# Kernel tuning notes

Measured on AMD Instinct MI355X. Metric: run time of the kernel, lower is better.

Reference implementation:

```python
import jax, jax.numpy as jnp
import numpy as np

B, S, D = 2, 2048, 2048
H = 16
HD = D // H  # 128
ROPE_THETA = 10000.0


def _rotate_half(x):
    # interleaved rotate: [-x2_0, x1_0, -x2_1, x1_1, ...]
    x1 = x[..., ::2]
    x2 = x[..., 1::2]
    return jnp.stack((-x2, x1), axis=-1).reshape(x.shape)


def _rope_cos_sin(seq_len, head_dim, dtype):
    inv_freq = 1.0 / (ROPE_THETA ** (jnp.arange(0, head_dim, 2, dtype=jnp.float32) / head_dim))
    pos = jnp.arange(seq_len, dtype=jnp.float32)
    freqs = pos[:, None] * inv_freq[None, :]          # [S, HD/2]
    angles = jnp.concatenate((freqs, freqs), axis=-1)  # [S, HD]  (matches torch.cat((freqs, freqs), -1))
    return jnp.cos(angles).astype(dtype), jnp.sin(angles).astype(dtype)


def setup_inputs() -> dict:
    key = jax.random.key(0)
    ks = jax.random.split(key, 5)
    scale = 1.0 / np.sqrt(D)
    return {
        "x": jax.random.normal(ks[0], (B, S, D), dtype=jnp.float32),
        "Wq": jax.random.normal(ks[1], (D, D), dtype=jnp.float32) * scale,
        "Wk": jax.random.normal(ks[2], (D, D), dtype=jnp.float32) * scale,
        "Wv": jax.random.normal(ks[3], (D, D), dtype=jnp.float32) * scale,
        "Wo": jax.random.normal(ks[4], (D, D), dtype=jnp.float32) * scale,
    }


def reference(x, Wq, Wk, Wv, Wo):
    b, s, d = x.shape
    # separate Q/K/V projections (no bias), reshape to [B, H, S, HD]
    def proj(W):
        return jnp.einsum('bsd,de->bse', x, W).reshape(b, s, H, HD).transpose(0, 2, 1, 3)
    q, k, v = proj(Wq), proj(Wk), proj(Wv)

    cos, sin = _rope_cos_sin(s, HD, q.dtype)  # [S, HD]
    cos = cos[None, None, :, :]
    sin = sin[None, None, :, :]
    q = q * cos + _rotate_half(q) * sin
    k = k * cos + _rotate_half(k) * sin

    # causal scaled dot-product attention
    scores = jnp.einsum('bhqd,bhkd->bhqk', q, k) / jnp.sqrt(jnp.asarray(HD, q.dtype))
    causal = jnp.tril(jnp.ones((s, s), dtype=bool))
    scores = jnp.where(causal[None, None, :, :], scores, jnp.asarray(-jnp.inf, scores.dtype))
    attn = jax.nn.softmax(scores, axis=-1)
    out = jnp.einsum('bhqk,bhkd->bhqd', attn, v)

    out = out.transpose(0, 2, 1, 3).reshape(b, s, d)
    return jnp.einsum('bsd,de->bse', out, Wo)
```

## Files before the change

kernel.cpp:

```cpp
#include <hip/hip_runtime.h>
#include <hip/hip_bf16.h>
#include <math.h>

typedef unsigned short u16;
typedef unsigned int u32;

#define Bz 2
#define Sz 2048
#define Dz 2048
#define Hz 16
#define HDz 128
#define Mz 4096

typedef __bf16 bf16x8 __attribute__((ext_vector_type(8)));
typedef float f32x4 __attribute__((ext_vector_type(4)));

__device__ __forceinline__ float bf2f(u16 h) {
    union { u32 u; float f; } x; x.u = ((u32)h) << 16; return x.f;
}
__device__ __forceinline__ u16 f2bf(float f) {
    union { float f; u32 u; } x; x.f = f;
    u32 u = x.u;
    return (u16)((u + 0x7FFFu + ((u >> 16) & 1u)) >> 16);
}
__device__ __forceinline__ u32 pack_bf16_trunc(float lo, float hi) {
    union { float f; u32 u; } a, b; a.f = lo; b.f = hi;
    return (a.u >> 16) | (b.u & 0xFFFF0000u);
}
__device__ __forceinline__ u32 pack_bf16_rn(float lo, float hi) {
    return (u32)f2bf(lo) | ((u32)f2bf(hi) << 16);
}
__device__ __forceinline__ float fexp2(float x) {
#if __has_builtin(__builtin_amdgcn_exp2f)
    return __builtin_amdgcn_exp2f(x);
#else
    return exp2f(x);
#endif
}
__device__ __forceinline__ void gl_lds16(const void* g, void* l) {
    __builtin_amdgcn_global_load_lds(
        (const __attribute__((address_space(1))) void*)g,
        (__attribute__((address_space(3))) void*)l, 16, 0, 0);
}

__global__ void cvt_f32_bf16(const float* __restrict__ src, u16* __restrict__ dst) {
    size_t i = (size_t)blockIdx.x * blockDim.x + threadIdx.x;
    float4 a = ((const float4*)src)[2 * i];
    float4 b = ((const float4*)src)[2 * i + 1];
    u16 r[8] = {f2bf(a.x), f2bf(a.y), f2bf(a.z), f2bf(a.w),
                f2bf(b.x), f2bf(b.y), f2bf(b.z), f2bf(b.w)};
    *(uint4*)(dst + 8 * i) = *(const uint4*)r;
}

__global__ void transpose_w(const float* __restrict__ W0, const float* __restrict__ W1,
                            const float* __restrict__ W2, const float* __restrict__ W3,
                            u16* __restrict__ Wt) {
    __shared__ u16 t[64][65];
    const float* src = (blockIdx.z == 0) ? W0 : (blockIdx.z == 1) ? W1
                     : (blockIdx.z == 2) ? W2 : W3;
    u16* dst = Wt + (size_t)blockIdx.z * (Dz * Dz);
    int x = blockIdx.x * 64, y = blockIdx.y * 64;
    int c = threadIdx.x & 63, rb = (threadIdx.x >> 6) * 16;
#pragma unroll
    for (int i = 0; i < 16; i++) {
        int r = rb + i;
        t[r][c] = f2bf(src[(size_t)(y + r) * Dz + x + c]);
    }
    __syncthreads();
#pragma unroll
    for (int i = 0; i < 16; i++) {
        int r = rb + i;
        dst[(size_t)(x + r) * Dz + y + c] = t[c][r];
    }
}

template <int MODE>
__global__ void gemm_bt(const u16* __restrict__ A, const u16* __restrict__ BtBase,
                        void* __restrict__ CBase) {
    const int z = blockIdx.z;
    const u16* Bt = BtBase + (size_t)z * (Dz * Dz);
    const int tid = threadIdx.x, lane = tid & 63, wave = tid >> 6;
    const int ln = lane & 15, qd = lane >> 4;
    const int m0 = blockIdx.y * 128, n0 = blockIdx.x * 128;

    __shared__ __align__(16) u16 As[128][64];
    __shared__ __align__(16) u16 Bs[128][64];

    f32x4 acc[4][4];
#pragma unroll
    for (int i = 0; i < 4; i++)
#pragma unroll
        for (int j = 0; j < 4; j++) acc[i][j] = (f32x4){0.f, 0.f, 0.f, 0.f};

    const int wm = (wave >> 1) * 64, wn = (wave & 1) * 64;
    const int lr8 = lane >> 3;
    const int bgo = (((lane & 7) ^ lr8) * 8);
    const int x7 = ln & 7;

    for (int k0 = 0; k0 < Dz; k0 += 64) {
        const u16* ga = A  + (size_t)(m0 + wave * 32 + lr8) * Dz + k0 + bgo;
        const u16* gb = Bt + (size_t)(n0 + wave * 32 + lr8) * Dz + k0 + bgo;
#pragma unroll
        for (int i = 0; i < 4; i++) {
            gl_lds16(ga + (size_t)(8 * i) * Dz, &As[wave * 32 + 8 * i][0]);
            gl_lds16(gb + (size_t)(8 * i) * Dz, &Bs[wave * 32 + 8 * i][0]);
        }
        __syncthreads();
#pragma unroll
        for (int kc = 0; kc < 2; kc++) {
            bf16x8 af[4], bff[4];
            const int cs = ((4 * kc + qd) ^ x7) * 8;
#pragma unroll
            for (int i = 0; i < 4; i++) {
                af[i]  = *(const bf16x8*)&As[wm + i * 16 + ln][cs];
                bff[i] = *(const bf16x8*)&Bs[wn + i * 16 + ln][cs];
            }
#pragma unroll
            for (int i = 0; i < 4; i++)
#pragma unroll
                for (int j = 0; j < 4; j++)
                    acc[i][j] = __builtin_amdgcn_mfma_f32_16x16x32_bf16(
                        af[i], bff[j], acc[i][j], 0, 0, 0);
        }
        __syncthreads();
    }

#pragma unroll
    for (int i = 0; i < 4; i++) {
#pragma unroll
        for (int j = 0; j < 4; j++) {
#pragma unroll
            for (int r = 0; r < 4; r++) {
                int row = m0 + wm + i * 16 + qd * 4 + r;
                int col = n0 + wn + j * 16 + ln;
                if (MODE == 0) {
                    ((float*)CBase)[(size_t)row * Dz + col] = acc[i][j][r];
                } else {
                    u16* C = (u16*)CBase + (size_t)z * ((size_t)Mz * Dz);
                    u16 hv = f2bf(acc[i][j][r]);
                    int bb = row >> 11, ss = row & 2047;
                    int hh = col >> 7, hd = col & 127;
                    if (z == 2)
                        C[((size_t)(bb * Hz + hh) * HDz + hd) * Sz + ss] = hv;
                    else
                        C[((size_t)(bb * Hz + hh) * Sz + ss) * HDz + hd] = hv;
                }
            }
        }
    }
}

__global__ void rope_kernel(u16* __restrict__ Q, u16* __restrict__ Kk) {
    u32 idx = blockIdx.x * blockDim.x + threadIdx.x;
    int isK = (idx >> 22) & 1;
    u16* T = isK ? Kk : Q;
    u32 p = idx & 0x3FFFFFu;
    int j = p & 63;
    int s = (p >> 6) & 2047;
    size_t base = (size_t)(p >> 6) * HDz + 2 * j;
    u32 u = *(u32*)(T + base);
    float x0 = bf2f((u16)(u & 0xFFFFu));
    float x1 = bf2f((u16)(u >> 16));
    int i0 = (2 * j) & 63;
    const float LG = 0.20762050593046017f;
    float f0 = exp2f(-LG * (float)i0);
    float f1 = exp2f(-LG * (float)(i0 + 1));
    float th0 = (float)s * f0, th1 = (float)s * f1;
    float s0, c0, s1, c1;
    sincosf(th0, &s0, &c0);
    sincosf(th1, &s1, &c1);
    float scl = isK ? 1.0f : 0.12751771218027603f;
    float y0 = (x0 * c0 - x1 * s0) * scl;
    float y1 = (x1 * c1 + x0 * s1) * scl;
    u32 outw = (u32)f2bf(y0) | ((u32)f2bf(y1) << 16);
    *(u32*)(T + base) = outw;
}

__global__ __launch_bounds__(256, 4)
void flash_attn(const u16* __restrict__ Q, const u16* __restrict__ Kk,
                const u16* __restrict__ Vt, u16* __restrict__ O) {
    const int tid = threadIdx.x, lane = tid & 63, wave = tid >> 6;
    const int ln = lane & 15, qd = lane >> 4;
    const int bh = blockIdx.x & 31;
    const int qt = 31 - (blockIdx.x >> 5);
    const int b = bh >> 4, h = bh & 15;
    const int q0 = qt * 64;
    const u16* Qh = Q  + (size_t)bh * Sz * HDz;
    const u16* Kh = Kk + (size_t)bh * Sz * HDz;
    const u16* Vh = Vt + (size_t)bh * HDz * Sz;

    __shared__ __align__(16) u16 Ks[64][128];
    __shared__ __align__(16) u16 Vs[144][64];

    for (int idx = tid; idx < 16 * 64; idx += 256) {
        int rr = idx >> 6, cc = idx & 63;
        Vs[128 + rr][cc] = (rr == 0) ? (u16)0x3F80 : (u16)0;
    }

    const int qabs = q0 + wave * 16 + ln;
    bf16x8 qf[4];
#pragma unroll
    for (int kc = 0; kc < 4; kc++) {
        uint4 t = *(const uint4*)(Qh + (size_t)qabs * HDz + kc * 32 + qd * 8);
        qf[kc] = *(const bf16x8*)&t;
    }

    float m_run = -INFINITY;
    f32x4 oa[9];
#pragma unroll
    for (int n = 0; n < 9; n++) oa[n] = (f32x4){0.f, 0.f, 0.f, 0.f};

    const int x7 = ln & 7;
    const int l4 = lane >> 4, c16 = lane & 15;
    const int lr8 = lane >> 3;
    const int bgv = ((lane & 7) ^ lr8) * 8;

    for (int k0 = 0; k0 <= q0; k0 += 64) {
        {
#pragma unroll
            for (int i = 0; i < 4; i++) {
                int rw = 4 * (i & 1) + l4;
                const u16* gk = Kh + (size_t)(k0 + 16 * wave + 4 * i + l4) * HDz
                                   + ((c16 ^ rw) * 8);
                gl_lds16(gk, &Ks[16 * wave + 4 * i][0]);
            }
            const u16* gv = Vh + (size_t)(32 * wave + lr8) * Sz + k0 + bgv;
#pragma unroll
            for (int i = 0; i < 4; i++)
                gl_lds16(gv + (size_t)(8 * i) * Sz, &Vs[32 * wave + 8 * i][0]);
        }
        __syncthreads();

        f32x4 sc4[4];
#pragma unroll
        for (int mt = 0; mt < 4; mt++) sc4[mt] = (f32x4){0.f, 0.f, 0.f, 0.f};
#pragma unroll
        for (int kc = 0; kc < 4; kc++) {
            const int cs = ((4 * kc + qd) ^ x7) * 8;
#pragma unroll
            for (int mt = 0; mt < 4; mt++) {
                bf16x8 kf = *(const bf16x8*)&Ks[mt * 16 + ln][cs];
                sc4[mt] = __builtin_amdgcn_mfma_f32_16x16x32_bf16(kf, qf[kc], sc4[mt], 0, 0, 0);
            }
        }
        if (k0 == q0) {
#pragma unroll
            for (int mt = 0; mt < 4; mt++)
#pragma unroll
                for (int r = 0; r < 4; r++)
                    if (mt * 16 + qd * 4 + r > 16 * wave + ln) sc4[mt][r] = -3e38f;
        }

        float rm = -3e38f;
#pragma unroll
        for (int mt = 0; mt < 4; mt++) {
            rm = fmaxf(rm, fmaxf(fmaxf(sc4[mt][0], sc4[mt][1]),
                                 fmaxf(sc4[mt][2], sc4[mt][3])));
        }
        rm = fmaxf(rm, __shfl_xor(rm, 16));
        rm = fmaxf(rm, __shfl_xor(rm, 32));
        float mn = fmaxf(m_run, rm);
        bool resc = (__ballot(mn > m_run) != 0ULL);
        float al = fexp2(m_run - mn);
        m_run = mn;
        if (resc) {
#pragma unroll
            for (int n = 0; n < 9; n++)
#pragma unroll
                for (int r = 0; r < 4; r++) oa[n][r] *= al;
        }

        u32 pku[8];
#pragma unroll
        for (int mt = 0; mt < 4; mt++) {
#pragma unroll
            for (int t = 0; t < 2; t++)
                pku[mt * 2 + t] = pack_bf16_trunc(fexp2(sc4[mt][2 * t] - mn),
                                                  fexp2(sc4[mt][2 * t + 1] - mn));
        }

#pragma unroll
        for (int kc = 0; kc < 2; kc++) {
            union { u32 w[4]; bf16x8 v; } pb;
#pragma unroll
            for (int s = 0; s < 4; s++) {
                int srcl = ((2 * (qd & 1) + (s >> 1)) << 4) | ln;
                u32 a0 = (u32)__shfl((int)pku[4 * kc + (s & 1)], srcl);
                u32 a1 = (u32)__shfl((int)pku[4 * kc + 2 + (s & 1)], srcl);
                pb.w[s] = (qd & 2) ? a1 : a0;
            }
            const int cs = ((4 * kc + qd) ^ x7) * 8;
#pragma unroll
            for (int mt = 0; mt < 9; mt++) {
                bf16x8 vf = *(const bf16x8*)&Vs[mt * 16 + ln][cs];
                oa[mt] = __builtin_amdgcn_mfma_f32_16x16x32_bf16(vf, pb.v, oa[mt], 0, 0, 0);
            }
        }
        __syncthreads();
    }

    float l = __shfl(oa[8][0], ln);
    float linv = 1.0f / l;
    u16* op = O + ((size_t)b * Sz + qabs) * Dz + h * HDz;
#pragma unroll
    for (int mt = 0; mt < 8; mt++) {
        u32 w0 = pack_bf16_rn(oa[mt][0] * linv, oa[mt][1] * linv);
        u32 w1 = pack_bf16_rn(oa[mt][2] * linv, oa[mt][3] * linv);
        uint2 ww; ww.x = w0; ww.y = w1;
        *(uint2*)(op + mt * 16 + qd * 4) = ww;
    }
}

extern "C" void kernel_launch(void* const* d_in, const int* in_sizes, int n_in,
                              void* d_out, int out_size, void* d_ws, size_t ws_size,
                              hipStream_t stream) {
    const float* x  = (const float*)d_in[0];
    const float* Wq = (const float*)d_in[1];
    const float* Wk = (const float*)d_in[2];
    const float* Wv = (const float*)d_in[3];
    const float* Wo = (const float*)d_in[4];
    u16* ws  = (u16*)d_ws;

    u16* wt = ws;
    u16* q  = ws + 16777216;
    u16* kk = q + 8388608;
    u16* v  = kk + 8388608;
    u16* xb = v + 8388608;
    u16* o  = xb;

    cvt_f32_bf16<<<dim3(4096), 256, 0, stream>>>(x, xb);
    transpose_w<<<dim3(32, 32, 4), 256, 0, stream>>>(Wq, Wk, Wv, Wo, wt);
    gemm_bt<1><<<dim3(16, 32, 3), 256, 0, stream>>>(xb, wt, q);
    rope_kernel<<<dim3(32768), 256, 0, stream>>>(q, kk);
    flash_attn<<<dim3(1024), 256, 0, stream>>>(q, kk, v, o);
    gemm_bt<0><<<dim3(16, 32, 1), 256, 0, stream>>>(o, wt + 3 * 4194304, (float*)d_out);
}
```

Measured before the change: 373.4 us.

## Use 256x256-tile 8-wave pipelined GEMM for the QKV projection

Replaces the QKV projection GEMM with a new kernel that uses 256x256 output tiles, 512 threads, and double-buffered LDS filled by direct global-to-LDS loads. The main loop is split into eight phases that interleave the next stage's loads with MFMA work, using explicit waitcnt, barriers and setprio. The goal is more data reuse per tile and better overlap of memory with compute. In exchange it uses more LDS and registers, and the launch grid shrinks to 384 blocks.

```diff
diff --git a/kernel.cpp b/kernel.cpp
--- a/kernel.cpp
+++ b/kernel.cpp
@@ -145,6 +145,123 @@
                     else
                         C[((size_t)(bb * Hz + hh) * Sz + ss) * HDz + hd] = hv;
                 }
+            }
+        }
+    }
+}
+
+#define G256_STAGE_A(BUF, MH, KOFS) do {                                        \
+    gl_lds16(gA0 + (size_t)(MH) * 64 * Dz + (KOFS), &As[BUF][sa0 + (MH) * 64][0]); \
+    gl_lds16(gA1 + (size_t)(MH) * 64 * Dz + (KOFS), &As[BUF][sa1 + (MH) * 64][0]); \
+} while (0)
+#define G256_STAGE_B(BUF, NH, KOFS) do {                                        \
+    gl_lds16(gB0 + (size_t)(NH) * 32 * Dz + (KOFS), &Bs[BUF][sb0 + (NH) * 32][0]); \
+    gl_lds16(gB1 + (size_t)(NH) * 32 * Dz + (KOFS), &Bs[BUF][sb1 + (NH) * 32][0]); \
+} while (0)
+#define G256_NOVM do {} while (0)
+#define G256_VM4  asm volatile("s_waitcnt vmcnt(4)" ::: "memory")
+#define G256_PHASE(BUF, MH, NH, STG, VMW) do {                                  \
+    bf16x8 af[4][2], bfr[2][2];                                                 \
+    _Pragma("unroll")                                                           \
+    for (int kc = 0; kc < 2; ++kc) {                                            \
+        const int cs = ((4 * kc + qd) ^ x7) * 8;                                \
+        _Pragma("unroll")                                                       \
+        for (int m = 0; m < 4; ++m)                                             \
+            af[m][kc] = *(const bf16x8*)&As[BUF][wr * 128 + (MH) * 64 + m * 16 + ln][cs]; \
+        _Pragma("unroll")                                                       \
+        for (int n = 0; n < 2; ++n)                                             \
+            bfr[n][kc] = *(const bf16x8*)&Bs[BUF][wc * 64 + (NH) * 32 + n * 16 + ln][cs]; \
+    }                                                                           \
+    STG;                                                                        \
+    asm volatile("s_waitcnt lgkmcnt(8)" ::: "memory");                          \
+    asm volatile("s_barrier" ::: "memory");                                     \
+    asm volatile("s_waitcnt lgkmcnt(0)" ::: "memory");                          \
+    __builtin_amdgcn_sched_barrier(0);                                          \
+    __builtin_amdgcn_s_setprio(1);                                              \
+    _Pragma("unroll")                                                           \
+    for (int kc = 0; kc < 2; ++kc)                                              \
+        _Pragma("unroll")                                                       \
+        for (int m = 0; m < 4; ++m)                                             \
+            _Pragma("unroll")                                                   \
+            for (int n = 0; n < 2; ++n)                                         \
+                acc[(MH) * 4 + m][(NH) * 2 + n] =                               \
+                    __builtin_amdgcn_mfma_f32_16x16x32_bf16(                    \
+                        af[m][kc], bfr[n][kc],                                  \
+                        acc[(MH) * 4 + m][(NH) * 2 + n], 0, 0, 0);              \
+    __builtin_amdgcn_s_setprio(0);                                              \
+    VMW;                                                                        \
+    asm volatile("s_barrier" ::: "memory");                                     \
+} while (0)
+
+__global__ __launch_bounds__(512, 2)
+void gemm256_qkv(const u16* __restrict__ A, const u16* __restrict__ BtBase,
+                 u16* __restrict__ CBase) {
+    const int z = blockIdx.z;
+    const u16* Bt = BtBase + (size_t)z * (Dz * Dz);
+    const int tid = threadIdx.x, lane = tid & 63, w = tid >> 6;
+    const int ln = lane & 15, qd = lane >> 4;
+    const int x7 = ln & 7;
+    const int wr = w >> 2, wc = w & 3;
+    const int m0 = blockIdx.y * 256, n0 = blockIdx.x * 256;
+
+    __shared__ __align__(16) u16 As[2][256][64];
+    __shared__ __align__(16) u16 Bs[2][256][64];
+
+    f32x4 acc[8][4];
+#pragma unroll
+    for (int i = 0; i < 8; ++i)
+#pragma unroll
+        for (int j = 0; j < 4; ++j) acc[i][j] = (f32x4){0.f, 0.f, 0.f, 0.f};
+
+    const int l8 = lane >> 3;
+    const int cblk = ((lane & 7) ^ l8) * 8;
+    const int sa0 = ((w >= 4) ? 128 : 0) + (((2 * w) & 7) * 8);
+    const int sa1 = ((w >= 4) ? 128 : 0) + (((2 * w + 1) & 7) * 8);
+    const int sb0 = (w >> 1) * 64 + (((2 * w) & 3) * 8);
+    const int sb1 = (w >> 1) * 64 + (((2 * w + 1) & 3) * 8);
+    const u16* gA0 = A + (size_t)(m0 + sa0 + l8) * Dz + cblk;
+    const u16* gA1 = A + (size_t)(m0 + sa1 + l8) * Dz + cblk;
+    const u16* gB0 = Bt + (size_t)(n0 + sb0 + l8) * Dz + cblk;
+    const u16* gB1 = Bt + (size_t)(n0 + sb1 + l8) * Dz + cblk;
+
+    G256_STAGE_A(0, 0, 0); G256_STAGE_A(0, 1, 0);
+    G256_STAGE_B(0, 0, 0); G256_STAGE_B(0, 1, 0);
+    G256_STAGE_A(1, 0, 64); G256_STAGE_B(1, 0, 64);
+    asm volatile("s_waitcnt vmcnt(4)" ::: "memory");
+    asm volatile("s_barrier" ::: "memory");
+
+#pragma unroll 1
+    for (int it = 0; it < Dz / 128; ++it) {
+        const int kb = it * 128;
+        const int k1 = kb + 64;
+        const int k2 = (kb + 128 < Dz) ? (kb + 128) : (Dz - 128);
+        const int k3 = (kb + 192 < Dz) ? (kb + 192) : (Dz - 64);
+        G256_PHASE(0, 0, 0, G256_STAGE_A(1, 1, k1), G256_NOVM);
+        G256_PHASE(0, 0, 1, G256_STAGE_B(1, 1, k1), G256_NOVM);
+        G256_PHASE(0, 1, 0, G256_STAGE_A(0, 0, k2), G256_NOVM);
+        G256_PHASE(0, 1, 1, G256_STAGE_B(0, 0, k2), G256_VM4);
+        G256_PHASE(1, 0, 0, G256_STAGE_A(0, 1, k2), G256_NOVM);
+        G256_PHASE(1, 0, 1, G256_STAGE_B(0, 1, k2), G256_NOVM);
+        G256_PHASE(1, 1, 0, G256_STAGE_A(1, 0, k3), G256_NOVM);
+        G256_PHASE(1, 1, 1, G256_STAGE_B(1, 0, k3), G256_VM4);
+    }
+
+    u16* C = CBase + (size_t)z * ((size_t)Mz * Dz);
+#pragma unroll
+    for (int i = 0; i < 8; ++i) {
+#pragma unroll
+        for (int j = 0; j < 4; ++j) {
+#pragma unroll
+            for (int r = 0; r < 4; ++r) {
+                int row = m0 + wr * 128 + i * 16 + qd * 4 + r;
+                int col = n0 + wc * 64 + j * 16 + ln;
+                u16 hv = f2bf(acc[i][j][r]);
+                int bb = row >> 11, ss = row & 2047;
+                int hh = col >> 7, hd = col & 127;
+                if (z == 2)
+                    C[((size_t)(bb * Hz + hh) * HDz + hd) * Sz + ss] = hv;
+                else
+                    C[((size_t)(bb * Hz + hh) * Sz + ss) * HDz + hd] = hv;
             }
         }
     }
@@ -330,7 +447,7 @@
 
     cvt_f32_bf16<<<dim3(4096), 256, 0, stream>>>(x, xb);
     transpose_w<<<dim3(32, 32, 4), 256, 0, stream>>>(Wq, Wk, Wv, Wo, wt);
-    gemm_bt<1><<<dim3(16, 32, 3), 256, 0, stream>>>(xb, wt, q);
+    gemm256_qkv<<<dim3(8, 16, 3), 512, 0, stream>>>(xb, wt, q);
     rope_kernel<<<dim3(32768), 256, 0, stream>>>(q, kk);
     flash_attn<<<dim3(1024), 256, 0, stream>>>(q, kk, v, o);
     gemm_bt<0><<<dim3(16, 32, 1), 256, 0, stream>>>(o, wt + 3 * 4194304, (float*)d_out);
```

Result: slower. 453.5 us (+21.4%).
